# Kernel optimization log

Hardware: AMD Instinct MI355X
Metric: run time of the kernel (lower is better)

Reference implementation:

```python
import jax, jax.numpy as jnp
import numpy as np

N_NODES = 50000
N_EDGES = 1600000
IN_CH = 128
HEADS = 4
OUT_CH = 32
NEG_SLOPE = 0.2
EPS = 1e-9


def setup_inputs() -> dict:
    key = jax.random.key(0)
    k_x, k_ei, k_w, k_as, k_ad = jax.random.split(key, 5)
    x = jax.random.normal(k_x, (N_NODES, IN_CH), dtype=jnp.float32)
    edge_index = jax.random.randint(k_ei, (2, N_EDGES), 0, N_NODES, dtype=jnp.int64)
    # xavier-uniform-like init for params
    wb = np.sqrt(6.0 / (IN_CH + HEADS * OUT_CH))
    weight = jax.random.uniform(k_w, (IN_CH, HEADS * OUT_CH), minval=-wb, maxval=wb, dtype=jnp.float32)
    ab = np.sqrt(6.0 / (HEADS + OUT_CH))
    att_src = jax.random.uniform(k_as, (HEADS, OUT_CH), minval=-ab, maxval=ab, dtype=jnp.float32)
    att_dst = jax.random.uniform(k_ad, (HEADS, OUT_CH), minval=-ab, maxval=ab, dtype=jnp.float32)
    bias = jnp.zeros((HEADS * OUT_CH,), dtype=jnp.float32)
    return {"x": x, "edge_index": edge_index, "weight": weight,
            "att_src": att_src, "att_dst": att_dst, "bias": bias}


def reference(x, edge_index, weight, att_src, att_dst, bias):
    N = x.shape[0]
    H, C = att_src.shape
    # add self loops
    loop = jnp.arange(N, dtype=edge_index.dtype)
    ei = jnp.concatenate([edge_index, jnp.stack([loop, loop], axis=0)], axis=1)
    src, dst = ei[0], ei[1]
    # linear projection -> [N, H, C]
    h = (x @ weight).reshape(N, H, C)
    # per-node attention logits, then gather per edge (same math as gathering h first)
    a_s = jnp.einsum('nhc,hc->nh', h, att_src)  # [N, H]
    a_d = jnp.einsum('nhc,hc->nh', h, att_dst)  # [N, H]
    scores = a_s[src] + a_d[dst]                # [E, H]
    scores = jnp.where(scores >= 0, scores, NEG_SLOPE * scores)  # leaky_relu
    # edge softmax over incoming edges of each dst node (all heads vectorized)
    mx = jax.ops.segment_max(scores, dst, num_segments=N)        # [N, H]
    ex = jnp.exp(scores - mx[dst])                               # [E, H]
    denom = jax.ops.segment_sum(ex, dst, num_segments=N)         # [N, H]
    alpha = ex / (denom[dst] + EPS)                              # [E, H]
    # weighted scatter-add aggregation
    msgs = alpha[:, :, None] * h[src]                            # [E, H, C]
    agg = jax.ops.segment_sum(msgs, dst, num_segments=N)         # [N, H, C]
    out = agg.reshape(N, H * C) + bias
    return out
```

## Files before the change

### kernel.cpp

```cpp
#include <hip/hip_runtime.h>

#define NN 50000
#define NE 1600000
#define IN_CH 128
#define HEADS 4
#define OUT_CH 32
#define HC 128
#define NEG_SLOPE 0.2f
#define EPS 1e-9f
#define SEG 96

#define FGRP 8
#define DPG (NN / FGRP)
#define FILL_BPG ((NE / 8 + 255) / 256)
#define ROWS_PB 64
#define PROJ_BLOCKS ((NN + ROWS_PB - 1) / ROWS_PB)
#define XPITCH 136

#define ENC_NEG_INF 0x007FFFFFu

using bf16x8 = __attribute__((ext_vector_type(8))) short;
using f32x4  = __attribute__((ext_vector_type(4))) float;
using u16x8  = __attribute__((ext_vector_type(8))) unsigned short;

__device__ __forceinline__ float leaky(float v) {
    return v >= 0.0f ? v : NEG_SLOPE * v;
}
__device__ __forceinline__ unsigned short f2bf(float f) {
    unsigned u = __float_as_uint(f);
    return (unsigned short)((u + 0x7fffu + ((u >> 16) & 1u)) >> 16);
}
__device__ __forceinline__ float bf2f(unsigned short b) {
    return __uint_as_float((unsigned)b << 16);
}
__device__ __forceinline__ unsigned int fenc(float f) {
    unsigned int u = __float_as_uint(f);
    return (u & 0x80000000u) ? ~u : (u | 0x80000000u);
}
__device__ __forceinline__ float fdec(unsigned int u) {
    return (u & 0x80000000u) ? __uint_as_float(u & 0x7fffffffu)
                             : __uint_as_float(~u);
}

__global__ __launch_bounds__(256) void k_init(unsigned int* __restrict__ gmax,
                                              const float* __restrict__ W,
                                              unsigned short* __restrict__ Wt_bf) {
    int i = blockIdx.x * 256 + threadIdx.x;
    if (i < HEADS) gmax[i] = ENC_NEG_INF;
    if (i < IN_CH * HC) {
        int k = i >> 7, n = i & 127;
        Wt_bf[n * IN_CH + k] = f2bf(W[i]);
    }
}

__global__ __launch_bounds__(256) void k_proj_fill(
        const float* __restrict__ x,
        const unsigned short* __restrict__ Wt_bf,
        const float* __restrict__ att_s, const float* __restrict__ att_d,
        unsigned short* __restrict__ h_bf,
        float* __restrict__ a_s, float* __restrict__ a_d,
        const int* __restrict__ ei, int* __restrict__ cnt,
        int* __restrict__ csr_src, unsigned int* __restrict__ gmax) {
    if (blockIdx.x >= PROJ_BLOCKS) {
        const int fb = blockIdx.x - PROJ_BLOCKS;
        const int f = fb & (FGRP - 1);
        const int bg = fb >> 3;
        const int e0 = (bg * 256 + (int)threadIdx.x) * 8;
        if (e0 >= NE) return;
        const int lo = f * DPG;
        const int4 d0 = *(const int4*)(ei + NE + e0);
        const int4 d1 = *(const int4*)(ei + NE + e0 + 4);
        const int4 s0 = *(const int4*)(ei + e0);
        const int4 s1 = *(const int4*)(ei + e0 + 4);
        const int d[8] = {d0.x, d0.y, d0.z, d0.w, d1.x, d1.y, d1.z, d1.w};
        const int s[8] = {s0.x, s0.y, s0.z, s0.w, s1.x, s1.y, s1.z, s1.w};
#pragma unroll
        for (int k = 0; k < 8; ++k) {
            if ((unsigned)(d[k] - lo) < (unsigned)DPG) {
                const int pos = atomicAdd(&cnt[d[k]], 1);
                if (pos < SEG)
                    csr_src[(size_t)d[k] * SEG + pos] = s[k];
            }
        }
        return;
    }
    __shared__ short xs[ROWS_PB * XPITCH];
    __shared__ float gsm[4][4];
    const int tid = threadIdx.x;
    const int n0 = blockIdx.x * ROWS_PB;

#pragma unroll
    for (int it = 0; it < 8; ++it) {
        const int idx = it * 256 + tid;
        const int row = idx >> 5;
        const int k4 = idx & 31;
        f32x4 v = {0.f, 0.f, 0.f, 0.f};
        if (n0 + row < NN)
            v = __builtin_nontemporal_load(
                    (const f32x4*)(x + (size_t)(n0 + row) * IN_CH + k4 * 4));
        short* p = &xs[row * XPITCH + k4 * 4];
        p[0] = (short)f2bf(v[0]); p[1] = (short)f2bf(v[1]);
        p[2] = (short)f2bf(v[2]); p[3] = (short)f2bf(v[3]);
    }
    __syncthreads();

    const int wave = tid >> 6;
    const int lane = tid & 63;
    const int quad = lane >> 4;
    const int m16 = lane & 15;
    const int wrow = wave * 16;

    bf16x8 a[4];
#pragma unroll
    for (int ks = 0; ks < 4; ++ks)
        a[ks] = *(const bf16x8*)&xs[(wrow + m16) * XPITCH + ks * 32 + quad * 8];

    const int row_base = n0 + wrow + quad * 4;
    float gmx[4];
#pragma unroll
    for (int hh = 0; hh < 4; ++hh) {
        float psh[4] = {0.f, 0.f, 0.f, 0.f};
        float pdh[4] = {0.f, 0.f, 0.f, 0.f};
#pragma unroll
        for (int c2 = 0; c2 < 2; ++c2) {
            const int ct = hh * 2 + c2;
            const unsigned short* wb = Wt_bf + (size_t)(ct * 16 + m16) * IN_CH + quad * 8;
            bf16x8 b0 = *(const bf16x8*)(wb);
            bf16x8 b1 = *(const bf16x8*)(wb + 32);
            bf16x8 b2 = *(const bf16x8*)(wb + 64);
            bf16x8 b3 = *(const bf16x8*)(wb + 96);
            f32x4 acc = {0.f, 0.f, 0.f, 0.f};
            acc = __builtin_amdgcn_mfma_f32_16x16x32_bf16(a[0], b0, acc, 0, 0, 0);
            acc = __builtin_amdgcn_mfma_f32_16x16x32_bf16(a[1], b1, acc, 0, 0, 0);
            acc = __builtin_amdgcn_mfma_f32_16x16x32_bf16(a[2], b2, acc, 0, 0, 0);
            acc = __builtin_amdgcn_mfma_f32_16x16x32_bf16(a[3], b3, acc, 0, 0, 0);
            const int col = ct * 16 + m16;
            const float asv = att_s[col];
            const float adv = att_d[col];
#pragma unroll
            for (int r = 0; r < 4; ++r) {
                const int n = row_base + r;
                if (n < NN) h_bf[(size_t)n * HC + col] = f2bf(acc[r]);
                psh[r] = fmaf(acc[r], asv, psh[r]);
                pdh[r] = fmaf(acc[r], adv, pdh[r]);
            }
        }
#pragma unroll
        for (int mk = 1; mk <= 8; mk <<= 1) {
#pragma unroll
            for (int r = 0; r < 4; ++r) {
                psh[r] += __shfl_xor(psh[r], mk, 64);
                pdh[r] += __shfl_xor(pdh[r], mk, 64);
            }
        }
        if (m16 == 0) {
#pragma unroll
            for (int r = 0; r < 4; ++r) {
                const int n = row_base + r;
                if (n < NN) {
                    a_s[n * HEADS + hh] = psh[r];
                    a_d[n * HEADS + hh] = pdh[r];
                }
            }
        }
        float mx = fmaxf(fmaxf(psh[0], psh[1]), fmaxf(psh[2], psh[3]));
        mx = fmaxf(mx, __shfl_xor(mx, 16, 64));
        mx = fmaxf(mx, __shfl_xor(mx, 32, 64));
        gmx[hh] = mx;
    }
    if (lane == 0) {
        gsm[wave][0] = gmx[0]; gsm[wave][1] = gmx[1];
        gsm[wave][2] = gmx[2]; gsm[wave][3] = gmx[3];
    }
    __syncthreads();
    if (tid < 4) {
        float mm = fmaxf(fmaxf(gsm[0][tid], gsm[1][tid]),
                         fmaxf(gsm[2][tid], gsm[3][tid]));
        atomicMax(&gmax[tid], fenc(mm));
    }
}

__global__ __launch_bounds__(256) void k_agg(const int* __restrict__ cnt,
                                             const int* __restrict__ csr_src,
                                             const unsigned short* __restrict__ h_bf,
                                             const float* __restrict__ a_s,
                                             const float* __restrict__ a_d,
                                             const unsigned int* __restrict__ gmax,
                                             const float* __restrict__ bias,
                                             float* __restrict__ out) {
    const int n = blockIdx.x * 4 + (threadIdx.x >> 6);
    const int lane = threadIdx.x & 63;
    if (n >= NN) return;
    const int q = lane >> 4;
    const int ql = lane & 15;
    const int hd = ql >> 2;
    int dg = cnt[n];
    if (dg > SEG) dg = SEG;
    const int beg = n * SEG;
    const int end = beg + dg;

    const float ad_h = a_d[n * 4 + hd];
    const float bound = leaky(fdec(gmax[hd]) + ad_h);

    float ev = 0.25f * __expf(leaky(a_s[n * 4 + hd] + ad_h) - bound);
    float denom = ev;
    const u16x8 hs = *(const u16x8*)(h_bf + (size_t)n * HC + 8 * ql);
    float acc[8];
#pragma unroll
    for (int k = 0; k < 8; ++k) acc[k] = ev * bf2f(hs[k]);

    int i = beg + q;
    int s0v = (i < end)     ? csr_src[i]     : n;
    int s1v = (i + 4 < end) ? csr_src[i + 4] : n;
    float as0 = a_s[s0v * 4 + hd];
    u16x8 hv0 = *(const u16x8*)(h_bf + (size_t)s0v * HC + 8 * ql);

    for (; i < end; i += 4) {
        const int s2v = (i + 8 < end) ? csr_src[i + 8] : n;
        const float as1 = a_s[s1v * 4 + hd];
        const u16x8 hv1 = *(const u16x8*)(h_bf + (size_t)s1v * HC + 8 * ql);
        const float e = __expf(leaky(as0 + ad_h) - bound);
        denom += e;
#pragma unroll
        for (int k = 0; k < 8; ++k)
            acc[k] = fmaf(e, bf2f(hv0[k]), acc[k]);
        as0 = as1; hv0 = hv1; s1v = s2v;
    }
#pragma unroll
    for (int k = 0; k < 8; ++k) {
        acc[k] += __shfl_xor(acc[k], 16, 64);
        acc[k] += __shfl_xor(acc[k], 32, 64);
    }
    denom += __shfl_xor(denom, 16, 64);
    denom += __shfl_xor(denom, 32, 64);

    if (q == 0) {
        const float inv = 1.0f / (denom + EPS);
        float* o = out + (size_t)n * HC + 8 * ql;
        const float* b = bias + 8 * ql;
        f32x4 o0, o1;
        o0[0] = acc[0] * inv + b[0]; o0[1] = acc[1] * inv + b[1];
        o0[2] = acc[2] * inv + b[2]; o0[3] = acc[3] * inv + b[3];
        o1[0] = acc[4] * inv + b[4]; o1[1] = acc[5] * inv + b[5];
        o1[2] = acc[6] * inv + b[6]; o1[3] = acc[7] * inv + b[7];
        __builtin_nontemporal_store(o0, (f32x4*)(o));
        __builtin_nontemporal_store(o1, (f32x4*)(o + 4));
    }
}

extern "C" void kernel_launch(void* const* d_in, const int* in_sizes, int n_in,
                              void* d_out, int out_size, void* d_ws, size_t ws_size,
                              hipStream_t stream) {
    const float* x     = (const float*)d_in[0];
    const int*   ei    = (const int*)d_in[1];
    const float* W     = (const float*)d_in[2];
    const float* att_s = (const float*)d_in[3];
    const float* att_d = (const float*)d_in[4];
    const float* bias  = (const float*)d_in[5];
    float* out = (float*)d_out;

    char* ws = (char*)d_ws;
    int*   cnt     = (int*)ws;    ws += (size_t)NN * 4;
    unsigned int* gmax = (unsigned int*)ws; ws += 64;
    int*   csr_src = (int*)ws;    ws += (size_t)NN * SEG * 4;
    unsigned short* h_bf = (unsigned short*)ws; ws += (size_t)NN * HC * 2;
    float* a_s     = (float*)ws;  ws += (size_t)NN * HEADS * 4;
    float* a_d     = (float*)ws;  ws += (size_t)NN * HEADS * 4;
    unsigned short* Wt_bf = (unsigned short*)ws; ws += (size_t)IN_CH * HC * 2;

    hipMemsetAsync(cnt, 0, (size_t)NN * 4, stream);
    k_init     <<<(IN_CH * HC + 255) / 256, 256, 0, stream>>>(gmax, W, Wt_bf);
    k_proj_fill<<<PROJ_BLOCKS + FGRP * FILL_BPG, 256, 0, stream>>>(
        x, Wt_bf, att_s, att_d, h_bf, a_s, a_d, ei, cnt, csr_src, gmax);
    k_agg      <<<(NN + 3) / 4, 256, 0, stream>>>(cnt, csr_src, h_bf, a_s, a_d,
                                                  gmax, bias, out);
}
```

Measured before the change: 228.2 us.

## Split CSR fill into bucketing pass and per-group scatter pass

The old fill made each of eight block groups read the whole edge list and keep only edges whose destination fell in its range. The new pass reads edges once, buckets them by destination group into packed 32-bit queues using shared-memory ranks and one global atomic per group per block. A second kernel then scatters each group's queue into the CSR. This removes the 8x redundant edge reads but adds a queue write/read round trip and an extra launch. It also relies on QCAP capacity and on source ids fitting in 16 bits, which fails for NN=50000 sources above 65535? (50000 fits). The x loads also lose their nontemporal hint.

```diff
diff --git a/kernel.cpp b/kernel.cpp
--- a/kernel.cpp
+++ b/kernel.cpp
@@ -12,10 +12,15 @@
 
 #define FGRP 8
 #define DPG (NN / FGRP)
-#define FILL_BPG ((NE / 8 + 255) / 256)
 #define ROWS_PB 64
 #define PROJ_BLOCKS ((NN + ROWS_PB - 1) / ROWS_PB)
 #define XPITCH 136
+
+#define FILLA_BLOCKS ((NE / 8 + 255) / 256)
+#define QCAP 210000
+#define FB_EPB 2048
+#define FB_BPG ((QCAP + FB_EPB - 1) / FB_EPB)
+#define FB_BLOCKS (FGRP * FB_BPG)
 
 #define ENC_NEG_INF 0x007FFFFFu
 
@@ -53,40 +58,53 @@
     }
 }
 
-__global__ __launch_bounds__(256) void k_proj_fill(
+__global__ __launch_bounds__(256) void k_proj_fillA(
         const float* __restrict__ x,
         const unsigned short* __restrict__ Wt_bf,
         const float* __restrict__ att_s, const float* __restrict__ att_d,
         unsigned short* __restrict__ h_bf,
         float* __restrict__ a_s, float* __restrict__ a_d,
-        const int* __restrict__ ei, int* __restrict__ cnt,
-        int* __restrict__ csr_src, unsigned int* __restrict__ gmax) {
+        const int* __restrict__ ei,
+        unsigned int* __restrict__ queue, int* __restrict__ qcnt,
+        unsigned int* __restrict__ gmax) {
+    const int tid = threadIdx.x;
     if (blockIdx.x >= PROJ_BLOCKS) {
+        __shared__ int lcnt[FGRP];
+        __shared__ int sbase[FGRP];
         const int fb = blockIdx.x - PROJ_BLOCKS;
-        const int f = fb & (FGRP - 1);
-        const int bg = fb >> 3;
-        const int e0 = (bg * 256 + (int)threadIdx.x) * 8;
-        if (e0 >= NE) return;
-        const int lo = f * DPG;
-        const int4 d0 = *(const int4*)(ei + NE + e0);
-        const int4 d1 = *(const int4*)(ei + NE + e0 + 4);
-        const int4 s0 = *(const int4*)(ei + e0);
-        const int4 s1 = *(const int4*)(ei + e0 + 4);
-        const int d[8] = {d0.x, d0.y, d0.z, d0.w, d1.x, d1.y, d1.z, d1.w};
-        const int s[8] = {s0.x, s0.y, s0.z, s0.w, s1.x, s1.y, s1.z, s1.w};
-#pragma unroll
-        for (int k = 0; k < 8; ++k) {
-            if ((unsigned)(d[k] - lo) < (unsigned)DPG) {
-                const int pos = atomicAdd(&cnt[d[k]], 1);
-                if (pos < SEG)
-                    csr_src[(size_t)d[k] * SEG + pos] = s[k];
+        const int e0 = (fb * 256 + tid) * 8;
+        const bool valid = e0 < NE;
+        if (tid < FGRP) lcnt[tid] = 0;
+        __syncthreads();
+        int rank[8], grp[8];
+        unsigned pk[8];
+        if (valid) {
+            const int4 d0 = *(const int4*)(ei + NE + e0);
+            const int4 d1 = *(const int4*)(ei + NE + e0 + 4);
+            const int4 s0 = *(const int4*)(ei + e0);
+            const int4 s1 = *(const int4*)(ei + e0 + 4);
+            const int d[8] = {d0.x, d0.y, d0.z, d0.w, d1.x, d1.y, d1.z, d1.w};
+            const int s[8] = {s0.x, s0.y, s0.z, s0.w, s1.x, s1.y, s1.z, s1.w};
+#pragma unroll
+            for (int k = 0; k < 8; ++k) {
+                const int g = d[k] / DPG;
+                grp[k] = g;
+                pk[k] = ((unsigned)(d[k] - g * DPG) << 16) | (unsigned)s[k];
+                rank[k] = atomicAdd(&lcnt[g], 1);
             }
+        }
+        __syncthreads();
+        if (tid < FGRP) sbase[tid] = atomicAdd(&qcnt[tid], lcnt[tid]);
+        __syncthreads();
+        if (valid) {
+#pragma unroll
+            for (int k = 0; k < 8; ++k)
+                queue[(size_t)grp[k] * QCAP + sbase[grp[k]] + rank[k]] = pk[k];
         }
         return;
     }
     __shared__ short xs[ROWS_PB * XPITCH];
     __shared__ float gsm[4][4];
-    const int tid = threadIdx.x;
     const int n0 = blockIdx.x * ROWS_PB;
 
 #pragma unroll
@@ -94,13 +112,12 @@
         const int idx = it * 256 + tid;
         const int row = idx >> 5;
         const int k4 = idx & 31;
-        f32x4 v = {0.f, 0.f, 0.f, 0.f};
+        float4 v = make_float4(0.f, 0.f, 0.f, 0.f);
         if (n0 + row < NN)
-            v = __builtin_nontemporal_load(
-                    (const f32x4*)(x + (size_t)(n0 + row) * IN_CH + k4 * 4));
+            v = *(const float4*)(x + (size_t)(n0 + row) * IN_CH + k4 * 4);
         short* p = &xs[row * XPITCH + k4 * 4];
-        p[0] = (short)f2bf(v[0]); p[1] = (short)f2bf(v[1]);
-        p[2] = (short)f2bf(v[2]); p[3] = (short)f2bf(v[3]);
+        p[0] = (short)f2bf(v.x); p[1] = (short)f2bf(v.y);
+        p[2] = (short)f2bf(v.z); p[3] = (short)f2bf(v.w);
     }
     __syncthreads();
 
@@ -177,6 +194,32 @@
         float mm = fmaxf(fmaxf(gsm[0][tid], gsm[1][tid]),
                          fmaxf(gsm[2][tid], gsm[3][tid]));
         atomicMax(&gmax[tid], fenc(mm));
+    }
+}
+
+__global__ __launch_bounds__(256) void k_fillB(const unsigned int* __restrict__ queue,
+                                               const int* __restrict__ qcnt,
+                                               int* __restrict__ cnt,
+                                               int* __restrict__ csr_src) {
+    const int f = blockIdx.x & (FGRP - 1);
+    const int j = blockIdx.x >> 3;
+    const int m = qcnt[f];
+    const int base = j * FB_EPB + (int)threadIdx.x * 8;
+    if (base >= m) return;
+    const unsigned int* qf = queue + (size_t)f * QCAP;
+    const uint4 w0 = *(const uint4*)(qf + base);
+    const uint4 w1 = *(const uint4*)(qf + base + 4);
+    const unsigned w[8] = {w0.x, w0.y, w0.z, w0.w, w1.x, w1.y, w1.z, w1.w};
+    const int lo = f * DPG;
+#pragma unroll
+    for (int k = 0; k < 8; ++k) {
+        if (base + k < m) {
+            const int s = (int)(w[k] & 0xFFFFu);
+            const int d = (int)(w[k] >> 16) + lo;
+            const int pos = atomicAdd(&cnt[d], 1);
+            if (pos < SEG)
+                csr_src[(size_t)d * SEG + pos] = s;
+        }
     }
 }
 
@@ -261,17 +304,20 @@
 
     char* ws = (char*)d_ws;
     int*   cnt     = (int*)ws;    ws += (size_t)NN * 4;
+    int*   qcnt    = (int*)ws;    ws += 64;
     unsigned int* gmax = (unsigned int*)ws; ws += 64;
     int*   csr_src = (int*)ws;    ws += (size_t)NN * SEG * 4;
     unsigned short* h_bf = (unsigned short*)ws; ws += (size_t)NN * HC * 2;
     float* a_s     = (float*)ws;  ws += (size_t)NN * HEADS * 4;
     float* a_d     = (float*)ws;  ws += (size_t)NN * HEADS * 4;
     unsigned short* Wt_bf = (unsigned short*)ws; ws += (size_t)IN_CH * HC * 2;
-
-    hipMemsetAsync(cnt, 0, (size_t)NN * 4, stream);
-    k_init     <<<(IN_CH * HC + 255) / 256, 256, 0, stream>>>(gmax, W, Wt_bf);
-    k_proj_fill<<<PROJ_BLOCKS + FGRP * FILL_BPG, 256, 0, stream>>>(
-        x, Wt_bf, att_s, att_d, h_bf, a_s, a_d, ei, cnt, csr_src, gmax);
-    k_agg      <<<(NN + 3) / 4, 256, 0, stream>>>(cnt, csr_src, h_bf, a_s, a_d,
-                                                  gmax, bias, out);
-}
+    unsigned int* queue = (unsigned int*)ws; ws += (size_t)FGRP * QCAP * 4;
+
+    hipMemsetAsync(cnt, 0, (size_t)NN * 4 + 64, stream);
+    k_init      <<<(IN_CH * HC + 255) / 256, 256, 0, stream>>>(gmax, W, Wt_bf);
+    k_proj_fillA<<<PROJ_BLOCKS + FILLA_BLOCKS, 256, 0, stream>>>(
+        x, Wt_bf, att_s, att_d, h_bf, a_s, a_d, ei, queue, qcnt, gmax);
+    k_fillB     <<<FB_BLOCKS, 256, 0, stream>>>(queue, qcnt, cnt, csr_src);
+    k_agg       <<<(NN + 3) / 4, 256, 0, stream>>>(cnt, csr_src, h_bf, a_s, a_d,
+                                                   gmax, bias, out);
+}
```

New measurement: 264.8 us. +16.0%, slower.
